# Kernel tuning notes

Hardware: AMD Instinct MI355X
Metric: run time of the kernel (lower is better)

Reference implementation:

```python
import jax, jax.numpy as jnp
import numpy as np

B, H, LK, D = 8, 16, 4096, 128


def setup_inputs() -> dict:
    key = jax.random.key(0)
    ks = jax.random.split(key, 9)
    s = 1.0 / np.sqrt(D)
    return {
        "Q": jax.random.normal(ks[0], (B, H, 1, D), dtype=jnp.float32),
        "K": jax.random.normal(ks[1], (B, H, LK, D), dtype=jnp.float32),
        "V": jax.random.normal(ks[2], (B, H, LK, D), dtype=jnp.float32),
        "mask": jax.random.randint(ks[3], (B, H, 1, LK), 0, 2, dtype=jnp.int32),
        "scale": 1,  # accepted but unused by the original forward
        "W_pre": jax.random.normal(ks[4], (D, D), dtype=jnp.float32) * s,
        "b_pre": jax.random.normal(ks[5], (D,), dtype=jnp.float32) * s,
        "W_q": jax.random.normal(ks[6], (D, D), dtype=jnp.float32) * s,
        "W_v": jax.random.normal(ks[7], (D, 1), dtype=jnp.float32) * s,
    }


def reference(Q, K, V, mask, scale, W_pre, b_pre, W_q, W_v):
    # precompute = linear_pre(K): [B,H,LK,D]
    pre = jnp.einsum("bhkd,de->bhke", K, W_pre) + b_pre
    # targetT = linear_q(Q): [B,H,1,D], broadcast-added over keys
    tq = jnp.einsum("bhqd,de->bhqe", Q, W_q)
    tmp = jnp.tanh(pre + tq)  # [B,H,LK,D]
    # energy = linear_v(tmp) reshaped to [B,H,1,LK]
    energy = jnp.einsum("bhkd,d->bhk", tmp, W_v[:, 0])[:, :, None, :]
    m = mask.astype(energy.dtype)
    energy = energy * (1.0 - m) + m * (-1e6)
    score = jax.nn.softmax(energy, axis=-1)  # [B,H,1,LK]
    context = jnp.matmul(score, V)  # [B,H,1,D]
    return (context, score, pre)
```

## Files before the change

### kernel.cpp

```cpp
#include <hip/hip_runtime.h>
#include <hip/hip_bf16.h>
#include <math.h>

#define B_   8
#define H_   16
#define BH_  (B_*H_)
#define LK_  4096
#define D_   128

#define SEG   16
#define KSEG  (LK_/SEG)

typedef __attribute__((ext_vector_type(8))) short bf16x8;
typedef __attribute__((ext_vector_type(4))) float f32x4;
typedef __attribute__((ext_vector_type(4))) unsigned int u32x4;

__device__ __forceinline__ float fast_tanh(float x) {
    float ax = fabsf(x);
    float e  = __expf(2.0f * ax);
    float r  = 1.0f - __fdividef(2.0f, e + 1.0f);
    return copysignf(r, x);
}

__device__ __forceinline__ unsigned int cvtpk(float lo, float hi) {
    unsigned int r;
    asm("v_cvt_pk_bf16_f32 %0, %1, %2" : "=v"(r) : "v"(lo), "v"(hi));
    return r;
}

__device__ __forceinline__ unsigned short cvt_hi(float x) {
    __hip_bfloat16 bh = __float2bfloat16(x);
    return __builtin_bit_cast(unsigned short, bh);
}

__device__ __forceinline__ void cvt8v(const f32x4 a, const f32x4 b, bf16x8& h, bf16x8& l) {
    unsigned int h0 = cvtpk(a[0], a[1]);
    unsigned int h1 = cvtpk(a[2], a[3]);
    unsigned int h2 = cvtpk(b[0], b[1]);
    unsigned int h3 = cvtpk(b[2], b[3]);
    float l0 = a[0] - __uint_as_float(h0 << 16);
    float l1 = a[1] - __uint_as_float(h0 & 0xFFFF0000u);
    float l2 = a[2] - __uint_as_float(h1 << 16);
    float l3 = a[3] - __uint_as_float(h1 & 0xFFFF0000u);
    float l4 = b[0] - __uint_as_float(h2 << 16);
    float l5 = b[1] - __uint_as_float(h2 & 0xFFFF0000u);
    float l6 = b[2] - __uint_as_float(h3 << 16);
    float l7 = b[3] - __uint_as_float(h3 & 0xFFFF0000u);
    u32x4 hv = {h0, h1, h2, h3};
    u32x4 lv = {cvtpk(l0, l1), cvtpk(l2, l3), cvtpk(l4, l5), cvtpk(l6, l7)};
    h = __builtin_bit_cast(bf16x8, hv);
    l = __builtin_bit_cast(bf16x8, lv);
}

__device__ __forceinline__ void gld_lds16(const void* g, void* l) {
    __builtin_amdgcn_global_load_lds(
        (const __attribute__((address_space(1))) unsigned int*)g,
        (__attribute__((address_space(3))) unsigned int*)l,
        16, 0, 0);
}

__global__ void pack_kernel(const float* __restrict__ Wpre,
                            unsigned short* __restrict__ Whi) {
    int idx  = blockIdx.x * 256 + threadIdx.x;
    int j    = idx & 7;
    int lane = (idx >> 3) & 63;
    int nt   = (idx >> 9) & 7;
    int ks   = idx >> 12;
    int k    = ks * 32 + (lane >> 4) * 8 + j;
    int n    = nt * 16 + (lane & 15);
    Whi[idx] = cvt_hi(Wpre[k * D_ + n]);
}

__global__ void tq_kernel(const float* __restrict__ Q,
                          const float* __restrict__ Wq,
                          float* __restrict__ tq) {
    int bh = blockIdx.x;
    int e  = threadIdx.x;
    const float* q = Q + bh * D_;
    float acc = 0.0f;
#pragma unroll 8
    for (int d = 0; d < D_; ++d)
        acc = fmaf(q[d], Wq[d * D_ + e], acc);
    tq[bh * D_ + e] = acc;
}

__global__ void __launch_bounds__(256, 3)
main_kernel(const float* __restrict__ K,
            const unsigned short* __restrict__ Whi,
            const float* __restrict__ bpre,
            const float* __restrict__ Wv,
            const float* __restrict__ tqg,
            float* __restrict__ pre_out,
            float* __restrict__ ep0,
            float* __restrict__ ep1) {
    const int t    = threadIdx.x;
    const int lane = t & 63;
    const int wv_  = t >> 6;
    const int kg   = wv_ & 1;
    const int eh   = wv_ >> 1;
    const int l15  = lane & 15;
    const int lg   = lane >> 4;
    const int bh   = blockIdx.y;
    const int kblk = blockIdx.x * 256;

    __shared__ float Klds[2][4096];

    const float* Kbh = K + (size_t)bh * LK_ * D_;

    bf16x8 wf[4][4];
#pragma unroll
    for (int ks = 0; ks < 4; ++ks)
#pragma unroll
        for (int et = 0; et < 4; ++et)
            wf[ks][et] = *(const bf16x8*)(Whi + (((size_t)ks * 8 + eh * 4 + et) * 64 + lane) * 8);

    auto stageK = [&](int s, int buf) {
#pragma unroll
        for (int i = 0; i < 4; ++i) {
            const int g4  = wv_ * 4 + i;
            const int kg2 = g4 >> 3, ks2 = (g4 >> 1) & 3, h2 = g4 & 1;
            const int row = kblk + s * 32 + kg2 * 16 + l15;
            const int col = lg * 8 + ks2 * 32 + h2 * 4;
            gld_lds16(Kbh + (size_t)row * D_ + col, &Klds[buf][g4 * 256]);
        }
    };

    stageK(0, 0);
    asm volatile("s_waitcnt vmcnt(0)\n\ts_barrier" ::: "memory");

#pragma unroll
    for (int s = 0; s < 8; ++s) {
        if (s < 7) stageK(s + 1, (s + 1) & 1);

        const float* kb = Klds[s & 1];
        f32x4 acc[4];
#pragma unroll
        for (int et = 0; et < 4; ++et)
            acc[et] = (f32x4){0.f, 0.f, 0.f, 0.f};

#pragma unroll
        for (int ks = 0; ks < 4; ++ks) {
            const int gbase = ((kg * 4 + ks) * 2) * 256 + lane * 4;
            f32x4 p0 = *(const f32x4*)(kb + gbase);
            f32x4 p1 = *(const f32x4*)(kb + gbase + 256);
            bf16x8 kh, kl;
            cvt8v(p0, p1, kh, kl);
#pragma unroll
            for (int et = 0; et < 4; ++et) {
                acc[et] = __builtin_amdgcn_mfma_f32_16x16x32_bf16(wf[ks][et], kh, acc[et], 0, 0, 0);
                acc[et] = __builtin_amdgcn_mfma_f32_16x16x32_bf16(wf[ks][et], kl, acc[et], 0, 0, 0);
            }
        }

        const int key = kblk + s * 32 + kg * 16 + l15;
        float* pb = pre_out + (size_t)bh * LK_ * D_ + (size_t)key * D_;
        float ep = 0.0f;
#pragma unroll
        for (int et = 0; et < 4; ++et) {
            const int e0 = eh * 64 + et * 16 + lg * 4;
            const float4 bp = *(const float4*)(bpre + e0);
            const float4 tq = *(const float4*)(tqg + bh * D_ + e0);
            const float4 wv = *(const float4*)(Wv + e0);
            f32x4 a = acc[et];
            f32x4 v;
            v[0] = a[0] + bp.x;
            v[1] = a[1] + bp.y;
            v[2] = a[2] + bp.z;
            v[3] = a[3] + bp.w;
            __builtin_nontemporal_store(v, (f32x4*)(pb + e0));
            ep = fmaf(fast_tanh(v[0] + tq.x), wv.x, ep);
            ep = fmaf(fast_tanh(v[1] + tq.y), wv.y, ep);
            ep = fmaf(fast_tanh(v[2] + tq.z), wv.z, ep);
            ep = fmaf(fast_tanh(v[3] + tq.w), wv.w, ep);
        }
        ep += __shfl_xor(ep, 16, 64);
        ep += __shfl_xor(ep, 32, 64);
        if (lg == 0) {
            float* epo = (eh == 0) ? ep0 : ep1;
            epo[(size_t)bh * LK_ + key] = ep;
        }
        asm volatile("s_waitcnt vmcnt(0) lgkmcnt(0)\n\ts_barrier" ::: "memory");
    }
}

__global__ void ml_kernel(const float* __restrict__ ep0,
                          const float* __restrict__ ep1,
                          const int* __restrict__ mask,
                          float* __restrict__ ml) {
    const int bh = blockIdx.x;
    const int t  = threadIdx.x;
    const float* e0 = ep0 + (size_t)bh * LK_;
    const float* e1 = ep1 + (size_t)bh * LK_;
    const int*   m  = mask + (size_t)bh * LK_;

    float mx = -1e30f;
    for (int k = t; k < LK_; k += 256) {
        float v = m[k] ? -1.0e6f : (e0[k] + e1[k]);
        mx = fmaxf(mx, v);
    }
#pragma unroll
    for (int off = 32; off > 0; off >>= 1)
        mx = fmaxf(mx, __shfl_xor(mx, off, 64));
    __shared__ float wmax[4];
    if ((t & 63) == 0) wmax[t >> 6] = mx;
    __syncthreads();
    mx = fmaxf(fmaxf(wmax[0], wmax[1]), fmaxf(wmax[2], wmax[3]));

    float sum = 0.0f;
    for (int k = t; k < LK_; k += 256) {
        float v = m[k] ? -1.0e6f : (e0[k] + e1[k]);
        sum += __expf(v - mx);
    }
#pragma unroll
    for (int off = 32; off > 0; off >>= 1)
        sum += __shfl_xor(sum, off, 64);
    __shared__ float wsum[4];
    if ((t & 63) == 0) wsum[t >> 6] = sum;
    __syncthreads();
    if (t == 0) {
        ml[bh * 2]     = mx;
        ml[bh * 2 + 1] = wsum[0] + wsum[1] + wsum[2] + wsum[3];
    }
}

__global__ void score_ctx_kernel(const float* __restrict__ ep1,
                                 const int* __restrict__ mask,
                                 const float* __restrict__ V,
                                 const float* __restrict__ ml,
                                 float* __restrict__ score_out,
                                 float* __restrict__ part) {
    const int seg = blockIdx.x;
    const int bh  = blockIdx.y;
    const int t   = threadIdx.x;
    const int k0  = seg * KSEG;

    __shared__ float sc[KSEG];
    __shared__ float pl[8][136];

    const float mx  = ml[bh * 2];
    const float inv = 1.0f / ml[bh * 2 + 1];

    {
        const size_t gi = (size_t)bh * LK_ + k0 + t;
        float v = mask[gi] ? -1.0e6f : (score_out[gi] + ep1[gi]);
        float s = __expf(v - mx) * inv;
        sc[t] = s;
        score_out[gi] = s;
    }
    __syncthreads();

    const int d4 = t & 31;
    const int g  = t >> 5;
    const float* Vb = V + ((size_t)bh * LK_ + k0) * D_ + d4 * 4;
    float4 a = make_float4(0.f, 0.f, 0.f, 0.f);
#pragma unroll 4
    for (int kk = g; kk < KSEG; kk += 8) {
        float4 vv = *(const float4*)(Vb + (size_t)kk * D_);
        float s = sc[kk];
        a.x = fmaf(s, vv.x, a.x);
        a.y = fmaf(s, vv.y, a.y);
        a.z = fmaf(s, vv.z, a.z);
        a.w = fmaf(s, vv.w, a.w);
    }
    *(float4*)&pl[g][d4 * 4] = a;
    __syncthreads();

    if (t < 128) {
        float s = 0.0f;
#pragma unroll
        for (int gg = 0; gg < 8; ++gg)
            s += pl[gg][t];
        part[((size_t)bh * SEG + seg) * D_ + t] = s;
    }
}

__global__ void combine_kernel(const float* __restrict__ part,
                               float* __restrict__ ctx) {
    const int bh = blockIdx.x;
    const int d  = threadIdx.x;
    float s = 0.0f;
#pragma unroll
    for (int g = 0; g < SEG; ++g)
        s += part[((size_t)bh * SEG + g) * D_ + d];
    ctx[bh * D_ + d] = s;
}

extern "C" void kernel_launch(void* const* d_in, const int* in_sizes, int n_in,
                              void* d_out, int out_size, void* d_ws, size_t ws_size,
                              hipStream_t stream) {
    const float* Q    = (const float*)d_in[0];
    const float* K    = (const float*)d_in[1];
    const float* V    = (const float*)d_in[2];
    const int*   mask = (const int*)  d_in[3];
    const float* Wpre = (const float*)d_in[5];
    const float* bpre = (const float*)d_in[6];
    const float* Wq   = (const float*)d_in[7];
    const float* Wv   = (const float*)d_in[8];

    float* out   = (float*)d_out;
    float* ctx   = out;
    float* score = out + (size_t)BH_ * D_;
    float* pre   = score + (size_t)BH_ * LK_;

    float* w    = (float*)d_ws;
    float* tq   = w;
    float* ml   = tq + (size_t)BH_ * D_;
    float* part = ml + 2 * BH_;
    unsigned short* Whi = (unsigned short*)(part + (size_t)BH_ * SEG * D_);
    float* ep1  = (float*)(Whi + 16384);

    hipLaunchKernelGGL(pack_kernel, dim3(64), dim3(256), 0, stream, Wpre, Whi);
    hipLaunchKernelGGL(tq_kernel, dim3(BH_), dim3(D_), 0, stream, Q, Wq, tq);
    hipLaunchKernelGGL(main_kernel, dim3(LK_ / 256, BH_), dim3(256), 0, stream,
                       K, Whi, bpre, Wv, tq, pre, score, ep1);
    hipLaunchKernelGGL(ml_kernel, dim3(BH_), dim3(256), 0, stream, score, ep1, mask, ml);
    hipLaunchKernelGGL(score_ctx_kernel, dim3(SEG, BH_), dim3(256), 0, stream,
                       ep1, mask, V, ml, score, part);
    hipLaunchKernelGGL(combine_kernel, dim3(BH_), dim3(D_), 0, stream, part, ctx);
}
```

Measured before the change: 237.4 us.

## Triple-buffer K staging with partial vmcnt waits and hoist per-channel constants

Moves from double to triple buffering of K tiles in LDS, prefetching two stages ahead. The per-stage barrier now waits on a partial vmcnt count instead of draining all outstanding memory ops, so the nontemporal pre stores and the in-flight loads can overlap with compute. The bias, tq and Wv vectors are loaded once into registers before the loop, and the lg==0 guard on the energy store is removed so every lane writes the same value redundantly. This costs more LDS, which may reduce occupancy, plus extra registers, and it depends on the hand-counted vmcnt values being correct for the store and load mix.

Result: faster. 202.8 us (-14.6%).

```diff
diff --git a/kernel.cpp b/kernel.cpp
--- a/kernel.cpp
+++ b/kernel.cpp
@@ -103,7 +103,7 @@
     const int bh   = blockIdx.y;
     const int kblk = blockIdx.x * 256;
 
-    __shared__ float Klds[2][4096];
+    __shared__ float Klds[3][4096];
 
     const float* Kbh = K + (size_t)bh * LK_ * D_;
 
@@ -113,6 +113,17 @@
 #pragma unroll
         for (int et = 0; et < 4; ++et)
             wf[ks][et] = *(const bf16x8*)(Whi + (((size_t)ks * 8 + eh * 4 + et) * 64 + lane) * 8);
+
+    float4 bpv[4], tqv[4], wvv[4];
+#pragma unroll
+    for (int et = 0; et < 4; ++et) {
+        const int e0 = eh * 64 + et * 16 + lg * 4;
+        bpv[et] = *(const float4*)(bpre + e0);
+        tqv[et] = *(const float4*)(tqg + bh * D_ + e0);
+        wvv[et] = *(const float4*)(Wv + e0);
+    }
+
+    float* epo = (eh == 0) ? ep0 : ep1;
 
     auto stageK = [&](int s, int buf) {
 #pragma unroll
@@ -126,13 +137,14 @@
     };
 
     stageK(0, 0);
-    asm volatile("s_waitcnt vmcnt(0)\n\ts_barrier" ::: "memory");
+    stageK(1, 1);
+    asm volatile("s_waitcnt vmcnt(4)\n\ts_barrier" ::: "memory");
 
 #pragma unroll
     for (int s = 0; s < 8; ++s) {
-        if (s < 7) stageK(s + 1, (s + 1) & 1);
-
-        const float* kb = Klds[s & 1];
+        if (s + 2 < 8) stageK(s + 2, (s + 2) % 3);
+
+        const float* kb = Klds[s % 3];
         f32x4 acc[4];
 #pragma unroll
         for (int et = 0; et < 4; ++et)
@@ -158,28 +170,24 @@
 #pragma unroll
         for (int et = 0; et < 4; ++et) {
             const int e0 = eh * 64 + et * 16 + lg * 4;
-            const float4 bp = *(const float4*)(bpre + e0);
-            const float4 tq = *(const float4*)(tqg + bh * D_ + e0);
-            const float4 wv = *(const float4*)(Wv + e0);
             f32x4 a = acc[et];
             f32x4 v;
-            v[0] = a[0] + bp.x;
-            v[1] = a[1] + bp.y;
-            v[2] = a[2] + bp.z;
-            v[3] = a[3] + bp.w;
+            v[0] = a[0] + bpv[et].x;
+            v[1] = a[1] + bpv[et].y;
+            v[2] = a[2] + bpv[et].z;
+            v[3] = a[3] + bpv[et].w;
             __builtin_nontemporal_store(v, (f32x4*)(pb + e0));
-            ep = fmaf(fast_tanh(v[0] + tq.x), wv.x, ep);
-            ep = fmaf(fast_tanh(v[1] + tq.y), wv.y, ep);
-            ep = fmaf(fast_tanh(v[2] + tq.z), wv.z, ep);
-            ep = fmaf(fast_tanh(v[3] + tq.w), wv.w, ep);
+            ep = fmaf(fast_tanh(v[0] + tqv[et].x), wvv[et].x, ep);
+            ep = fmaf(fast_tanh(v[1] + tqv[et].y), wvv[et].y, ep);
+            ep = fmaf(fast_tanh(v[2] + tqv[et].z), wvv[et].z, ep);
+            ep = fmaf(fast_tanh(v[3] + tqv[et].w), wvv[et].w, ep);
         }
         ep += __shfl_xor(ep, 16, 64);
         ep += __shfl_xor(ep, 32, 64);
-        if (lg == 0) {
-            float* epo = (eh == 0) ? ep0 : ep1;
-            epo[(size_t)bh * LK_ + key] = ep;
-        }
-        asm volatile("s_waitcnt vmcnt(0) lgkmcnt(0)\n\ts_barrier" ::: "memory");
+        epo[(size_t)bh * LK_ + key] = ep;
+
+        if (s < 7)
+            asm volatile("s_waitcnt vmcnt(9)\n\ts_barrier" ::: "memory");
     }
 }
 
```
